# Performance work log

Hardware: AMD Instinct MI355X
Metric: run time of the kernel (lower is better)

## Reference

```python
import jax, jax.numpy as jnp
import numpy as np

M = 512          # feature_dim
NH = 8           # num_heads
FFN = 2048       # ffn_hidden_dim
NMOD = 4         # modalities (seq len for attention)
EPS = 1e-5


def setup_inputs() -> dict:
    key = jax.random.key(0)
    ks = jax.random.split(key, 16)
    B, H = 64, 256
    s = 0.02
    return {
        "x_image": jax.random.normal(ks[0], (B, H, M), jnp.float32),
        "x_radar": jax.random.normal(ks[1], (B, H, M), jnp.float32),
        "x_lidar": jax.random.normal(ks[2], (B, H, M), jnp.float32),
        "x_gps":   jax.random.normal(ks[3], (B, H, M), jnp.float32),
        # nn.MultiheadAttention params (torch layout: weight is (out,in))
        "in_proj_w": jax.random.normal(ks[4], (3 * M, M), jnp.float32) * s,
        "in_proj_b": jnp.zeros((3 * M,), jnp.float32),
        "out_proj_w": jax.random.normal(ks[5], (M, M), jnp.float32) * s,
        "out_proj_b": jnp.zeros((M,), jnp.float32),
        "ln1_g": jnp.ones((M,), jnp.float32),
        "ln1_b": jnp.zeros((M,), jnp.float32),
        "w1": jax.random.normal(ks[6], (FFN, M), jnp.float32) * s,
        "b1": jnp.zeros((FFN,), jnp.float32),
        "w2": jax.random.normal(ks[7], (M, FFN), jnp.float32) * s,
        "b2": jnp.zeros((M,), jnp.float32),
        "ln2_g": jnp.ones((M,), jnp.float32),
        "ln2_b": jnpp if False else jnp.zeros((M,), jnp.float32),
    }


def _layernorm(x, g, b):
    mu = jnp.mean(x, axis=-1, keepdims=True)
    var = jnp.mean((x - mu) ** 2, axis=-1, keepdims=True)
    return (x - mu) * jax.lax.rsqrt(var + EPS) * g + b


def _forward(x_image, x_radar, x_lidar, x_gps,
             in_proj_w, in_proj_b, out_proj_w, out_proj_b,
             ln1_g, ln1_b, w1, b1, w2, b2, ln2_g, ln2_b):
    B, H, _ = x_image.shape
    # F: (B*H, NMOD, M) -- fold batch and time; per-t loop is independent
    F = jnp.stack([x_image, x_radar, x_lidar, x_gps], axis=2).reshape(B * H, NMOD, M)
    qkv = F @ in_proj_w.T + in_proj_b              # (N, NMOD, 3M)
    q, k, v = jnp.split(qkv, 3, axis=-1)
    dh = M // NH
    def heads(t):  # (N, NMOD, M) -> (N, NH, NMOD, dh)
        return t.reshape(-1, NMOD, NH, dh).transpose(0, 2, 1, 3)
    qh, kh, vh = heads(q), heads(k), heads(v)
    scores = jnp.einsum("bhsd,bhtd->bhst", qh, kh) / np.sqrt(dh).astype(np.float32)
    attn = jax.nn.softmax(scores, axis=-1)
    o = jnp.einsum("bhst,bhtd->bhsd", attn, vh)
    o = o.transpose(0, 2, 1, 3).reshape(-1, NMOD, M)
    attn_out = o @ out_proj_w.T + out_proj_b
    h1 = _layernorm(F + attn_out, ln1_g, ln1_b)    # (N, NMOD, M)
    agg = h1.sum(axis=1)                            # (N, M)
    ffn = jax.nn.gelu(agg @ w1.T + b1, approximate=False) @ w2.T + b2
    z = _layernorm(agg + ffn, ln2_g, ln2_b)
    return z.reshape(B, H, M)


def reference(x_image, x_radar, x_lidar, x_gps,
              in_proj_w, in_proj_b, out_proj_w, out_proj_b,
              ln1_g, ln1_b, w1, b1, w2, b2, ln2_g, ln2_b):
    return _forward(x_image, x_radar, x_lidar, x_gps,
                    in_proj_w, in_proj_b, out_proj_w, out_proj_b,
                    ln1_g, ln1_b, w1, b1, w2, b2, ln2_g, ln2_b)
```

## Files before the change

kernel.cpp:

```cpp
#include <hip/hip_runtime.h>
#include <hip/hip_bf16.h>


typedef __attribute__((ext_vector_type(8))) short s16x8;
typedef __attribute__((ext_vector_type(4))) float f32x4;

__device__ __forceinline__ unsigned short f2bf(float f) {
  unsigned int u = __float_as_uint(f);
  u += 0x7fffu + ((u >> 16) & 1u);
  return (unsigned short)(u >> 16);
}
__device__ __forceinline__ float bf2f(unsigned short s) {
  return __uint_as_float(((unsigned int)s) << 16);
}
__device__ __forceinline__ f32x4 mfma16(s16x8 a, s16x8 b, f32x4 c) {
  return __builtin_amdgcn_mfma_f32_16x16x32_bf16(a, b, c, 0, 0, 0);
}
__device__ __forceinline__ int swz(int row, int bir) {
  return row * 128 + ((((row) & 7) << 4) ^ bir);
}
__device__ __forceinline__ int qkswz(int row, int c) {
  return row * 128 + ((((c >> 3) ^ (row & 7)) << 4)) + (c & 7) * 2;
}
__device__ __forceinline__ int vtswz(int d, int row) {
  return d * 256 + ((((row >> 3) ^ (d & 7)) << 4)) + (row & 7) * 2;
}
__device__ __forceinline__ int pwswz(int row, int c) {
  return row * 64 + ((((c >> 3) ^ (row & 3)) << 4)) + (c & 7) * 2;
}
__device__ __forceinline__ int vtoff(int r, int c) {
  return r * 1024 + ((c * 2) ^ ((r & 7) << 4));
}
__device__ __forceinline__ void gl_lds16(const void* g, void* l) {
  __builtin_amdgcn_global_load_lds(
      (const __attribute__((address_space(1))) unsigned int*)g,
      (__attribute__((address_space(3))) unsigned int*)l, 16, 0, 0);
}

__global__ void pack_kernel(const float* __restrict__ wqkv, const float* __restrict__ wout,
                            const float* __restrict__ w1, const float* __restrict__ w2,
                            const float* __restrict__ x0, const float* __restrict__ x1,
                            const float* __restrict__ x2, const float* __restrict__ x3,
                            unsigned short* __restrict__ o_wqkv, unsigned short* __restrict__ o_wout,
                            unsigned short* __restrict__ o_w1, unsigned short* __restrict__ o_w2,
                            unsigned short* __restrict__ o_x4) {
  const long c0 = 196608, c1 = 262144, c2 = 524288, c3 = 786432, c4 = 9175040;
  for (long v = (long)blockIdx.x * blockDim.x + threadIdx.x; v < c4;
       v += (long)gridDim.x * blockDim.x) {
    const float* src;
    unsigned short* dst;
    if (v < c0) { src = wqkv + v * 4; dst = o_wqkv + v * 4; }
    else if (v < c1) { long u = v - c0; src = wout + u * 4; dst = o_wout + u * 4; }
    else if (v < c2) { long u = v - c1; src = w1 + u * 4; dst = o_w1 + u * 4; }
    else if (v < c3) { long u = v - c2; src = w2 + u * 4; dst = o_w2 + u * 4; }
    else {
      long u = v - c3; long e = u * 4; long r = e >> 9; int i = (int)(e & 511);
      int s = (int)(r & 3); long n = r >> 2;
      const float* xs = (s == 0) ? x0 : (s == 1) ? x1 : (s == 2) ? x2 : x3;
      src = xs + n * 512 + i; dst = o_x4 + e;
    }
    float4 f = *reinterpret_cast<const float4*>(src);
    ushort4 hb;
    hb.x = f2bf(f.x); hb.y = f2bf(f.y); hb.z = f2bf(f.z); hb.w = f2bf(f.w);
    *reinterpret_cast<ushort4*>(dst) = hb;
  }
}

__launch_bounds__(256, 3)
__global__ void qkv_attn_kernel(const unsigned short* __restrict__ x4,
                                const unsigned short* __restrict__ wqkv,
                                const float* __restrict__ in_b,
                                unsigned short* __restrict__ o_out) {
  const int wg = blockIdx.x;
  const int slot = wg >> 3, xcd = wg & 7;
  const int tb = ((slot >> 3) << 3) | xcd;
  const int h = slot & 7;
  const int tid = threadIdx.x, lane = tid & 63, w = tid >> 6;
  const int wm = w >> 1, wn = w & 1;

  __shared__ __align__(16) unsigned char smem[49152];
  unsigned short* aT = (unsigned short*)smem;
  unsigned short* bT = (unsigned short*)(smem + 16384);
  unsigned short* Qs = (unsigned short*)smem;
  unsigned short* Ks = (unsigned short*)(smem + 16384);
  unsigned short* Vt = (unsigned short*)(smem + 32768);
  unsigned short* Pw = (unsigned short*)smem;
  unsigned short* outT = (unsigned short*)(smem + 16384);

  f32x4 acc[4][6];
#pragma unroll
  for (int i = 0; i < 4; ++i)
#pragma unroll
    for (int j = 0; j < 6; ++j) acc[i][j] = (f32x4){0.f, 0.f, 0.f, 0.f};

  const long rowBase = (long)tb * 128;
  const int loff = ((lane >> 3) * 512) + (((lane & 7) ^ (lane >> 3)) * 8);

  for (int kk = 0; kk < 8; ++kk) {
    const int k0 = kk * 64;
#pragma unroll
    for (int it = 0; it < 4; ++it) {
      int c = w * 4 + it;
      gl_lds16(x4 + (rowBase + c * 8) * 512 + k0 + loff, aT + c * 512);
    }
#pragma unroll
    for (int it = 0; it < 6; ++it) {
      int c = w * 6 + it;
      int bc0 = c * 8;
      int wb = (bc0 < 64) ? (h * 64 + bc0)
             : (bc0 < 128) ? (512 + h * 64 + (bc0 - 64))
                           : (1024 + h * 64 + (bc0 - 128));
      gl_lds16(wqkv + (long)wb * 512 + k0 + loff, bT + c * 512);
    }
    __syncthreads();
#pragma unroll
    for (int k2 = 0; k2 < 2; ++k2) {
      s16x8 af[4], bfr[6];
      const int bir = k2 * 64 + ((lane >> 4) << 4);
#pragma unroll
      for (int mi = 0; mi < 4; ++mi) {
        int row = wm * 64 + mi * 16 + (lane & 15);
        af[mi] = *(const s16x8*)((unsigned char*)aT + swz(row, bir));
      }
#pragma unroll
      for (int ni = 0; ni < 6; ++ni) {
        int col = wn * 96 + ni * 16 + (lane & 15);
        bfr[ni] = *(const s16x8*)((unsigned char*)bT + swz(col, bir));
      }
#pragma unroll
      for (int mi = 0; mi < 4; ++mi)
#pragma unroll
        for (int ni = 0; ni < 6; ++ni)
          acc[mi][ni] = mfma16(af[mi], bfr[ni], acc[mi][ni]);
    }
    __syncthreads();
  }

#pragma unroll
  for (int mi = 0; mi < 4; ++mi)
#pragma unroll
    for (int ni = 0; ni < 6; ++ni) {
      int col = wn * 96 + ni * 16 + (lane & 15);
      int wb = (col < 64) ? (h * 64 + col)
             : (col < 128) ? (512 + h * 64 + (col - 64))
                           : (1024 + h * 64 + (col - 128));
      float bias = in_b[wb];
      int row0 = wm * 64 + mi * 16 + ((lane >> 4) << 2);
#pragma unroll
      for (int r = 0; r < 4; ++r) {
        int row = row0 + r;
        unsigned short hv = f2bf(acc[mi][ni][r] + bias);
        if (col < 64)
          *(unsigned short*)((unsigned char*)Qs + qkswz(row, col)) = hv;
        else if (col < 128)
          *(unsigned short*)((unsigned char*)Ks + qkswz(row, col - 64)) = hv;
        else
          *(unsigned short*)((unsigned char*)Vt + vtswz(col - 128, row)) = hv;
      }
    }
  __syncthreads();

  f32x4 sacc[2];
#pragma unroll
  for (int i2 = 0; i2 < 2; ++i2) {
    int ti = w * 2 + i2;
    int qrow = ti * 16 + (lane & 15);
    int bir = (lane >> 4) << 4;
    s16x8 qa0 = *(const s16x8*)((unsigned char*)Qs + swz(qrow, bir));
    s16x8 qa1 = *(const s16x8*)((unsigned char*)Qs + swz(qrow, 64 + bir));
    s16x8 ka0 = *(const s16x8*)((unsigned char*)Ks + swz(qrow, bir));
    s16x8 ka1 = *(const s16x8*)((unsigned char*)Ks + swz(qrow, 64 + bir));
    f32x4 s = (f32x4){0.f, 0.f, 0.f, 0.f};
    s = mfma16(qa0, ka0, s);
    s = mfma16(qa1, ka1, s);
    sacc[i2] = s;
  }
  __syncthreads();
  {
    s16x8 z = (s16x8){0, 0, 0, 0, 0, 0, 0, 0};
    ((s16x8*)Pw)[tid] = z;
    ((s16x8*)Pw)[tid + 256] = z;
  }
  __syncthreads();

  const bool rel = ((lane & 15) >> 2) == (lane >> 4);
#pragma unroll
  for (int i2 = 0; i2 < 2; ++i2) {
    int ti = w * 2 + i2;
#pragma unroll
    for (int r = 0; r < 4; ++r) {
      float sc = sacc[i2][r] * 0.125f;
      float m = fmaxf(sc, __shfl_xor(sc, 1));
      m = fmaxf(m, __shfl_xor(m, 2));
      float e = __expf(sc - m);
      float su = e + __shfl_xor(e, 1);
      su = su + __shfl_xor(su, 2);
      float p = e / su;
      if (rel) {
        int row = ti * 16 + ((lane >> 4) << 2) + r;
        int cl = (((row >> 2) & 7) << 2) + (lane & 3);
        *(unsigned short*)((unsigned char*)Pw + pwswz(row, cl)) = f2bf(p);
      }
    }
  }
  __syncthreads();

#pragma unroll
  for (int i2 = 0; i2 < 2; ++i2) {
    int ti = w * 2 + i2;
    int arow = ti * 16 + (lane & 15);
    s16x8 pa = *(const s16x8*)((unsigned char*)Pw + arow * 64 +
                               ((((lane >> 4) ^ (arow & 3)) << 4)));
    f32x4 pv4[4];
#pragma unroll
    for (int n = 0; n < 4; ++n) {
      int d = n * 16 + (lane & 15);
      int gran = ((ti >> 1) << 2) + (lane >> 4);
      s16x8 vb = *(const s16x8*)((unsigned char*)Vt + d * 256 +
                                 (((gran ^ (d & 7)) << 4)));
      pv4[n] = mfma16(pa, vb, (f32x4){0.f, 0.f, 0.f, 0.f});
    }
#pragma unroll
    for (int n = 0; n < 4; ++n) {
      int d = n * 16 + (lane & 15);
      int row0 = ti * 16 + ((lane >> 4) << 2);
#pragma unroll
      for (int r = 0; r < 4; ++r)
        *(unsigned short*)((unsigned char*)outT + qkswz(row0 + r, d)) =
            f2bf(pv4[n][r]);
    }
  }
  __syncthreads();
#pragma unroll
  for (int j = 0; j < 4; ++j) {
    int c = j * 256 + tid;
    int row = c >> 3, ch = c & 7;
    s16x8 v = *(const s16x8*)((unsigned char*)outT + qkswz(row, ch * 8));
    *(s16x8*)(o_out + (rowBase + row) * 512 + h * 64 + ch * 8) = v;
  }
}

__launch_bounds__(256)
__global__ void outproj_ln1_kernel(const unsigned short* __restrict__ o_in,
                                   const unsigned short* __restrict__ wout,
                                   const float* __restrict__ out_b,
                                   const unsigned short* __restrict__ x4,
                                   const float* __restrict__ ln1_g, const float* __restrict__ ln1_b,
                                   float* __restrict__ agg_f, unsigned short* __restrict__ agg_b) {
  const int tb = blockIdx.x;
  const int tid = threadIdx.x, lane = tid & 63, w = tid >> 6;
  __shared__ __align__(16) unsigned char smem[53504];
  unsigned short* vt = (unsigned short*)smem;
  unsigned short* aT = (unsigned short*)(smem + 32768);
  unsigned short* bT = (unsigned short*)(smem + 36864);
  float* stats = (float*)(smem + 53248);
  const long rowBase = (long)tb * 32;

  for (int ns = 0; ns < 4; ++ns) {
    f32x4 acc[2][2];
#pragma unroll
    for (int i = 0; i < 2; ++i)
#pragma unroll
      for (int j = 0; j < 2; ++j) acc[i][j] = (f32x4){0.f, 0.f, 0.f, 0.f};
    for (int kk = 0; kk < 8; ++kk) {
      const int k0 = kk * 64;
      {
        int lr = tid >> 3, c8 = tid & 7;
        s16x8 v = *(const s16x8*)(o_in + (rowBase + lr) * 512 + k0 + c8 * 8);
        *(s16x8*)((unsigned char*)aT + swz(lr, c8 * 16)) = v;
      }
#pragma unroll
      for (int it = 0; it < 4; ++it) {
        int cid = tid + it * 256, bc = cid >> 3, c8 = cid & 7;
        s16x8 v = *(const s16x8*)(wout + (long)(ns * 128 + bc) * 512 + k0 + c8 * 8);
        *(s16x8*)((unsigned char*)bT + swz(bc, c8 * 16)) = v;
      }
      __syncthreads();
#pragma unroll
      for (int k2 = 0; k2 < 2; ++k2) {
        s16x8 af[2], bfr[2];
        const int bir = k2 * 64 + ((lane >> 4) << 4);
#pragma unroll
        for (int mi = 0; mi < 2; ++mi) {
          int row = mi * 16 + (lane & 15);
          af[mi] = *(const s16x8*)((unsigned char*)aT + swz(row, bir));
        }
#pragma unroll
        for (int ni = 0; ni < 2; ++ni) {
          int col = w * 32 + ni * 16 + (lane & 15);
          bfr[ni] = *(const s16x8*)((unsigned char*)bT + swz(col, bir));
        }
#pragma unroll
        for (int mi = 0; mi < 2; ++mi)
#pragma unroll
          for (int ni = 0; ni < 2; ++ni)
            acc[mi][ni] = mfma16(af[mi], bfr[ni], acc[mi][ni]);
      }
      __syncthreads();
    }
#pragma unroll
    for (int mi = 0; mi < 2; ++mi)
#pragma unroll
      for (int ni = 0; ni < 2; ++ni) {
        int gcol = ns * 128 + w * 32 + ni * 16 + (lane & 15);
        float bias = out_b[gcol];
        int row0 = mi * 16 + ((lane >> 4) << 2);
#pragma unroll
        for (int r = 0; r < 4; ++r) {
          int rr = row0 + r;
          float F = bf2f(x4[(rowBase + rr) * 512 + gcol]);
          *(unsigned short*)((unsigned char*)vt + vtoff(rr, gcol)) =
              f2bf(acc[mi][ni][r] + bias + F);
        }
      }
  }
  __syncthreads();
  {
    int wv = tid >> 6, ln = tid & 63;
    for (int i = 0; i < 8; ++i) {
      int r = wv * 8 + i;
      s16x8 v8 = *(const s16x8*)((unsigned char*)vt + vtoff(r, ln * 8));
      float sum = 0.f, sq = 0.f;
#pragma unroll
      for (int d = 0; d < 8; ++d) {
        float v = bf2f((unsigned short)v8[d]);
        sum += v; sq += v * v;
      }
#pragma unroll
      for (int off = 1; off < 64; off <<= 1) {
        sum += __shfl_xor(sum, off); sq += __shfl_xor(sq, off);
      }
      if (ln == 0) {
        float mu = sum * (1.f / 512.f);
        float var = sq * (1.f / 512.f) - mu * mu;
        stats[r * 2] = mu;
        stats[r * 2 + 1] = rsqrtf(var + 1e-5f);
      }
    }
  }
  __syncthreads();
  for (int it = 0; it < 2; ++it) {
    int ci = tid + it * 256;
    int tok = ci >> 6, c0 = (ci & 63) * 8;
    long gtok = (long)tb * 8 + tok;
    float a[8] = {0.f, 0.f, 0.f, 0.f, 0.f, 0.f, 0.f, 0.f};
#pragma unroll
    for (int s = 0; s < 4; ++s) {
      int r = tok * 4 + s;
      s16x8 v8 = *(const s16x8*)((unsigned char*)vt + vtoff(r, c0));
      float mu = stats[r * 2], is = stats[r * 2 + 1];
#pragma unroll
      for (int d = 0; d < 8; ++d) a[d] += (bf2f((unsigned short)v8[d]) - mu) * is;
    }
    float4 g0 = *(const float4*)(ln1_g + c0);
    float4 g1 = *(const float4*)(ln1_g + c0 + 4);
    float4 b0 = *(const float4*)(ln1_b + c0);
    float4 b1 = *(const float4*)(ln1_b + c0 + 4);
    float ov[8];
    ov[0] = g0.x * a[0] + 4.f * b0.x; ov[1] = g0.y * a[1] + 4.f * b0.y;
    ov[2] = g0.z * a[2] + 4.f * b0.z; ov[3] = g0.w * a[3] + 4.f * b0.w;
    ov[4] = g1.x * a[4] + 4.f * b1.x; ov[5] = g1.y * a[5] + 4.f * b1.y;
    ov[6] = g1.z * a[6] + 4.f * b1.z; ov[7] = g1.w * a[7] + 4.f * b1.w;
    *(float4*)(agg_f + gtok * 512 + c0) = (float4){ov[0], ov[1], ov[2], ov[3]};
    *(float4*)(agg_f + gtok * 512 + c0 + 4) = (float4){ov[4], ov[5], ov[6], ov[7]};
    s16x8 ab;
#pragma unroll
    for (int d = 0; d < 8; ++d) ab[d] = (short)f2bf(ov[d]);
    *(s16x8*)(agg_b + gtok * 512 + c0) = ab;
  }
}

__launch_bounds__(256)
__global__ void ffn1_kernel(const unsigned short* __restrict__ aggb,
                            const unsigned short* __restrict__ w1b,
                            const float* __restrict__ b1,
                            unsigned short* __restrict__ hidden) {
  const int wg = blockIdx.x;
  const int slot = wg >> 3, xcd = wg & 7;
  const int by = ((slot >> 4) << 3) | xcd;
  const int bx = slot & 15;
  const int tid = threadIdx.x, lane = tid & 63, w = tid >> 6;
  const int wm = w >> 1, wn = w & 1;
  __shared__ __align__(16) unsigned char smem[32768];
  unsigned short* aT = (unsigned short*)smem;
  unsigned short* bT = (unsigned short*)(smem + 16384);
  f32x4 acc[4][4];
#pragma unroll
  for (int i = 0; i < 4; ++i)
#pragma unroll
    for (int j = 0; j < 4; ++j) acc[i][j] = (f32x4){0.f, 0.f, 0.f, 0.f};
  const long rowBase = (long)by * 128;
  const long colBase = (long)bx * 128;
  const int loff = ((lane >> 3) * 512) + (((lane & 7) ^ (lane >> 3)) * 8);
  for (int kk = 0; kk < 8; ++kk) {
    const int k0 = kk * 64;
#pragma unroll
    for (int it = 0; it < 4; ++it) {
      int c = w * 4 + it;
      gl_lds16(aggb + (rowBase + c * 8) * 512 + k0 + loff, aT + c * 512);
    }
#pragma unroll
    for (int it = 0; it < 4; ++it) {
      int c = w * 4 + it;
      gl_lds16(w1b + (colBase + c * 8) * 512 + k0 + loff, bT + c * 512);
    }
    __syncthreads();
#pragma unroll
    for (int k2 = 0; k2 < 2; ++k2) {
      s16x8 af[4], bfr[4];
      const int bir = k2 * 64 + ((lane >> 4) << 4);
#pragma unroll
      for (int mi = 0; mi < 4; ++mi) {
        int row = wm * 64 + mi * 16 + (lane & 15);
        af[mi] = *(const s16x8*)((unsigned char*)aT + swz(row, bir));
      }
#pragma unroll
      for (int ni = 0; ni < 4; ++ni) {
        int col = wn * 64 + ni * 16 + (lane & 15);
        bfr[ni] = *(const s16x8*)((unsigned char*)bT + swz(col, bir));
      }
#pragma unroll
      for (int mi = 0; mi < 4; ++mi)
#pragma unroll
        for (int ni = 0; ni < 4; ++ni)
          acc[mi][ni] = mfma16(af[mi], bfr[ni], acc[mi][ni]);
    }
    __syncthreads();
  }
#pragma unroll
  for (int mi = 0; mi < 4; ++mi)
#pragma unroll
    for (int ni = 0; ni < 4; ++ni) {
      long gcol = colBase + wn * 64 + ni * 16 + (lane & 15);
      float bias = b1[gcol];
      int row0 = wm * 64 + mi * 16 + ((lane >> 4) << 2);
#pragma unroll
      for (int r = 0; r < 4; ++r) {
        float x = acc[mi][ni][r] + bias;
        float g = 0.5f * x * (1.f + erff(x * 0.70710678118f));
        hidden[(rowBase + row0 + r) * 2048 + gcol] = f2bf(g);
      }
    }
}

__launch_bounds__(256)
__global__ void ffn2_kernel(const unsigned short* __restrict__ hidden,
                            const unsigned short* __restrict__ w2b,
                            const float* __restrict__ b2,
                            const float* __restrict__ agg_f,
                            float* __restrict__ ffn2s) {
  const int wg = blockIdx.x;
  const int slot = wg >> 3, xcd = wg & 7;
  const int by = ((slot >> 2) << 3) | xcd;
  const int bx = slot & 3;
  const int tid = threadIdx.x, lane = tid & 63, w = tid >> 6;
  const int wm = w >> 1, wn = w & 1;
  __shared__ __align__(16) unsigned char smem[32768];
  unsigned short* aT = (unsigned short*)smem;
  unsigned short* bT = (unsigned short*)(smem + 16384);
  f32x4 acc[4][4];
#pragma unroll
  for (int i = 0; i < 4; ++i)
#pragma unroll
    for (int j = 0; j < 4; ++j) acc[i][j] = (f32x4){0.f, 0.f, 0.f, 0.f};
  const long rowBase = (long)by * 128;
  const long colBase = (long)bx * 128;
  const int loff2k = ((lane >> 3) * 2048) + (((lane & 7) ^ (lane >> 3)) * 8);
  for (int kk = 0; kk < 32; ++kk) {
    const int k0 = kk * 64;
#pragma unroll
    for (int it = 0; it < 4; ++it) {
      int c = w * 4 + it;
      gl_lds16(hidden + (rowBase + c * 8) * 2048 + k0 + loff2k, aT + c * 512);
    }
#pragma unroll
    for (int it = 0; it < 4; ++it) {
      int c = w * 4 + it;
      gl_lds16(w2b + (colBase + c * 8) * 2048 + k0 + loff2k, bT + c * 512);
    }
    __syncthreads();
#pragma unroll
    for (int k2 = 0; k2 < 2; ++k2) {
      s16x8 af[4], bfr[4];
      const int bir = k2 * 64 + ((lane >> 4) << 4);
#pragma unroll
      for (int mi = 0; mi < 4; ++mi) {
        int row = wm * 64 + mi * 16 + (lane & 15);
        af[mi] = *(const s16x8*)((unsigned char*)aT + swz(row, bir));
      }
#pragma unroll
      for (int ni = 0; ni < 4; ++ni) {
        int col = wn * 64 + ni * 16 + (lane & 15);
        bfr[ni] = *(const s16x8*)((unsigned char*)bT + swz(col, bir));
      }
#pragma unroll
      for (int mi = 0; mi < 4; ++mi)
#pragma unroll
        for (int ni = 0; ni < 4; ++ni)
          acc[mi][ni] = mfma16(af[mi], bfr[ni], acc[mi][ni]);
    }
    __syncthreads();
  }
#pragma unroll
  for (int mi = 0; mi < 4; ++mi)
#pragma unroll
    for (int ni = 0; ni < 4; ++ni) {
      long gcol = colBase + wn * 64 + ni * 16 + (lane & 15);
      float bias = b2[gcol];
      int row0 = wm * 64 + mi * 16 + ((lane >> 4) << 2);
#pragma unroll
      for (int r = 0; r < 4; ++r) {
        long grow = rowBase + row0 + r;
        ffn2s[grow * 512 + gcol] = acc[mi][ni][r] + bias + agg_f[grow * 512 + gcol];
      }
    }
}

__launch_bounds__(256)
__global__ void ln2_kernel(const float* __restrict__ ffn2s,
                           const float* __restrict__ ln2_g,
                           const float* __restrict__ ln2_b,
                           float* __restrict__ out) {
  const int tb = blockIdx.x;
  const int lane = threadIdx.x & 63, wv = threadIdx.x >> 6;
  const int c0 = lane * 8;
  float4 g0 = *(const float4*)(ln2_g + c0);
  float4 g1 = *(const float4*)(ln2_g + c0 + 4);
  float4 b0 = *(const float4*)(ln2_b + c0);
  float4 b1 = *(const float4*)(ln2_b + c0 + 4);
#pragma unroll
  for (int i = 0; i < 4; ++i) {
    long row = (long)tb * 16 + wv * 4 + i;
    const float* src = ffn2s + row * 512 + c0;
    float4 a = *(const float4*)src;
    float4 c = *(const float4*)(src + 4);
    float sum = a.x + a.y + a.z + a.w + c.x + c.y + c.z + c.w;
    float sq = a.x * a.x + a.y * a.y + a.z * a.z + a.w * a.w +
               c.x * c.x + c.y * c.y + c.z * c.z + c.w * c.w;
#pragma unroll
    for (int off = 1; off < 64; off <<= 1) {
      sum += __shfl_xor(sum, off); sq += __shfl_xor(sq, off);
    }
    float mu = sum * (1.f / 512.f);
    float is = rsqrtf(sq * (1.f / 512.f) - mu * mu + 1e-5f);
    float* dst = out + row * 512 + c0;
    *(float4*)dst = (float4){(a.x - mu) * is * g0.x + b0.x, (a.y - mu) * is * g0.y + b0.y,
                             (a.z - mu) * is * g0.z + b0.z, (a.w - mu) * is * g0.w + b0.w};
    *(float4*)(dst + 4) = (float4){(c.x - mu) * is * g1.x + b1.x, (c.y - mu) * is * g1.y + b1.y,
                                   (c.z - mu) * is * g1.z + b1.z, (c.w - mu) * is * g1.w + b1.w};
  }
}

extern "C" void kernel_launch(void* const* d_in, const int* in_sizes, int n_in,
                              void* d_out, int out_size, void* d_ws, size_t ws_size,
                              hipStream_t stream) {
  (void)in_sizes; (void)n_in; (void)out_size;
  const float* x0 = (const float*)d_in[0];
  const float* x1 = (const float*)d_in[1];
  const float* x2 = (const float*)d_in[2];
  const float* x3 = (const float*)d_in[3];
  const float* in_w = (const float*)d_in[4];
  const float* in_b = (const float*)d_in[5];
  const float* out_w = (const float*)d_in[6];
  const float* out_b = (const float*)d_in[7];
  const float* ln1_g = (const float*)d_in[8];
  const float* ln1_b = (const float*)d_in[9];
  const float* w1 = (const float*)d_in[10];
  const float* b1 = (const float*)d_in[11];
  const float* w2 = (const float*)d_in[12];
  const float* b2 = (const float*)d_in[13];
  const float* ln2_g = (const float*)d_in[14];
  const float* ln2_b = (const float*)d_in[15];
  float* out = (float*)d_out;

  unsigned char* ws = (unsigned char*)d_ws;
  if (ws_size < 190840832u) return;
  unsigned short* wqkv_b = (unsigned short*)(ws + 0);
  unsigned short* wout_b = (unsigned short*)(ws + 1572864);
  unsigned short* w1_b = (unsigned short*)(ws + 2097152);
  unsigned short* w2_b = (unsigned short*)(ws + 4194304);
  unsigned short* x4 = (unsigned short*)(ws + 6291456);
  unsigned short* o_buf = (unsigned short*)(ws + 73400320);
  float* agg_f = (float*)(ws + 140509184);
  unsigned short* agg_b = (unsigned short*)(ws + 174063616);
  unsigned short* hidden = o_buf;
  float* ffn2s = (float*)(ws + 6291456);

  pack_kernel<<<2048, 256, 0, stream>>>(in_w, out_w, w1, w2, x0, x1, x2, x3,
                                        wqkv_b, wout_b, w1_b, w2_b, x4);
  qkv_attn_kernel<<<4096, 256, 0, stream>>>(x4, wqkv_b, in_b, o_buf);
  outproj_ln1_kernel<<<2048, 256, 0, stream>>>(o_buf, wout_b, out_b, x4,
                                               ln1_g, ln1_b, agg_f, agg_b);
  ffn1_kernel<<<2048, 256, 0, stream>>>(agg_b, w1_b, b1, hidden);
  ffn2_kernel<<<512, 256, 0, stream>>>(hidden, w2_b, b2, agg_f, ffn2s);
  ln2_kernel<<<1024, 256, 0, stream>>>(ffn2s, ln2_g, ln2_b, out);
}
```

Baseline: 394.6 us.

## Fuse input fp32-to-bf16 conversion into QKV attention load and drop x4 buffer

Removes packing of the four modality inputs into an interleaved bf16 buffer. The QKV/attention kernel now reads fp32 inputs directly and converts to bf16 while staging into LDS, and the out-projection epilogue reads the fp32 residual directly. This saves a full write and read pass over a large intermediate. In exchange, each head block re-reads twice as many bytes per x tile, and the x loads become synchronous register loads instead of direct-to-LDS loads.

```diff
diff --git a/kernel.cpp b/kernel.cpp
--- a/kernel.cpp
+++ b/kernel.cpp
@@ -37,28 +37,19 @@
       (__attribute__((address_space(3))) unsigned int*)l, 16, 0, 0);
 }
 
-__global__ void pack_kernel(const float* __restrict__ wqkv, const float* __restrict__ wout,
-                            const float* __restrict__ w1, const float* __restrict__ w2,
-                            const float* __restrict__ x0, const float* __restrict__ x1,
-                            const float* __restrict__ x2, const float* __restrict__ x3,
-                            unsigned short* __restrict__ o_wqkv, unsigned short* __restrict__ o_wout,
-                            unsigned short* __restrict__ o_w1, unsigned short* __restrict__ o_w2,
-                            unsigned short* __restrict__ o_x4) {
-  const long c0 = 196608, c1 = 262144, c2 = 524288, c3 = 786432, c4 = 9175040;
-  for (long v = (long)blockIdx.x * blockDim.x + threadIdx.x; v < c4;
+__global__ void pack_w_kernel(const float* __restrict__ wqkv, const float* __restrict__ wout,
+                              const float* __restrict__ w1, const float* __restrict__ w2,
+                              unsigned short* __restrict__ o_wqkv, unsigned short* __restrict__ o_wout,
+                              unsigned short* __restrict__ o_w1, unsigned short* __restrict__ o_w2) {
+  const long c0 = 196608, c1 = 262144, c2 = 524288, c3 = 786432;
+  for (long v = (long)blockIdx.x * blockDim.x + threadIdx.x; v < c3;
        v += (long)gridDim.x * blockDim.x) {
     const float* src;
     unsigned short* dst;
     if (v < c0) { src = wqkv + v * 4; dst = o_wqkv + v * 4; }
     else if (v < c1) { long u = v - c0; src = wout + u * 4; dst = o_wout + u * 4; }
     else if (v < c2) { long u = v - c1; src = w1 + u * 4; dst = o_w1 + u * 4; }
-    else if (v < c3) { long u = v - c2; src = w2 + u * 4; dst = o_w2 + u * 4; }
-    else {
-      long u = v - c3; long e = u * 4; long r = e >> 9; int i = (int)(e & 511);
-      int s = (int)(r & 3); long n = r >> 2;
-      const float* xs = (s == 0) ? x0 : (s == 1) ? x1 : (s == 2) ? x2 : x3;
-      src = xs + n * 512 + i; dst = o_x4 + e;
-    }
+    else { long u = v - c2; src = w2 + u * 4; dst = o_w2 + u * 4; }
     float4 f = *reinterpret_cast<const float4*>(src);
     ushort4 hb;
     hb.x = f2bf(f.x); hb.y = f2bf(f.y); hb.z = f2bf(f.z); hb.w = f2bf(f.w);
@@ -67,7 +58,8 @@
 }
 
 __launch_bounds__(256, 3)
-__global__ void qkv_attn_kernel(const unsigned short* __restrict__ x4,
+__global__ void qkv_attn_kernel(const float* __restrict__ x0, const float* __restrict__ x1,
+                                const float* __restrict__ x2, const float* __restrict__ x3,
                                 const unsigned short* __restrict__ wqkv,
                                 const float* __restrict__ in_b,
                                 unsigned short* __restrict__ o_out) {
@@ -94,15 +86,12 @@
     for (int j = 0; j < 6; ++j) acc[i][j] = (f32x4){0.f, 0.f, 0.f, 0.f};
 
   const long rowBase = (long)tb * 128;
+  const long tokBase = (long)tb * 32;
   const int loff = ((lane >> 3) * 512) + (((lane & 7) ^ (lane >> 3)) * 8);
+  const float* xs[4] = {x0, x1, x2, x3};
 
   for (int kk = 0; kk < 8; ++kk) {
     const int k0 = kk * 64;
-#pragma unroll
-    for (int it = 0; it < 4; ++it) {
-      int c = w * 4 + it;
-      gl_lds16(x4 + (rowBase + c * 8) * 512 + k0 + loff, aT + c * 512);
-    }
 #pragma unroll
     for (int it = 0; it < 6; ++it) {
       int c = w * 6 + it;
@@ -111,6 +100,21 @@
              : (bc0 < 128) ? (512 + h * 64 + (bc0 - 64))
                            : (1024 + h * 64 + (bc0 - 128));
       gl_lds16(wqkv + (long)wb * 512 + k0 + loff, bT + c * 512);
+    }
+#pragma unroll
+    for (int it = 0; it < 4; ++it) {
+      int cid = tid + it * 256, lr = cid >> 3, c8 = cid & 7;
+      int s = lr & 3;
+      long n = tokBase + (lr >> 2);
+      const float* src = xs[s] + n * 512 + k0 + c8 * 8;
+      float4 f0 = *(const float4*)src;
+      float4 f1 = *(const float4*)(src + 4);
+      s16x8 v;
+      v[0] = (short)f2bf(f0.x); v[1] = (short)f2bf(f0.y);
+      v[2] = (short)f2bf(f0.z); v[3] = (short)f2bf(f0.w);
+      v[4] = (short)f2bf(f1.x); v[5] = (short)f2bf(f1.y);
+      v[6] = (short)f2bf(f1.z); v[7] = (short)f2bf(f1.w);
+      *(s16x8*)((unsigned char*)aT + swz(lr, c8 * 16)) = v;
     }
     __syncthreads();
 #pragma unroll
@@ -244,7 +248,8 @@
 __global__ void outproj_ln1_kernel(const unsigned short* __restrict__ o_in,
                                    const unsigned short* __restrict__ wout,
                                    const float* __restrict__ out_b,
-                                   const unsigned short* __restrict__ x4,
+                                   const float* __restrict__ x0, const float* __restrict__ x1,
+                                   const float* __restrict__ x2, const float* __restrict__ x3,
                                    const float* __restrict__ ln1_g, const float* __restrict__ ln1_b,
                                    float* __restrict__ agg_f, unsigned short* __restrict__ agg_b) {
   const int tb = blockIdx.x;
@@ -255,6 +260,7 @@
   unsigned short* bT = (unsigned short*)(smem + 36864);
   float* stats = (float*)(smem + 53248);
   const long rowBase = (long)tb * 32;
+  const float* xs[4] = {x0, x1, x2, x3};
 
   for (int ns = 0; ns < 4; ++ns) {
     f32x4 acc[2][2];
@@ -308,7 +314,9 @@
 #pragma unroll
         for (int r = 0; r < 4; ++r) {
           int rr = row0 + r;
-          float F = bf2f(x4[(rowBase + rr) * 512 + gcol]);
+          long grow = rowBase + rr;
+          int s = (int)(grow & 3); long n = grow >> 2;
+          float F = xs[s][n * 512 + gcol];
           *(unsigned short*)((unsigned char*)vt + vtoff(rr, gcol)) =
               f2bf(acc[mi][ni][r] + bias + F);
         }
@@ -579,17 +587,16 @@
   unsigned short* wout_b = (unsigned short*)(ws + 1572864);
   unsigned short* w1_b = (unsigned short*)(ws + 2097152);
   unsigned short* w2_b = (unsigned short*)(ws + 4194304);
-  unsigned short* x4 = (unsigned short*)(ws + 6291456);
+  float* ffn2s = (float*)(ws + 6291456);
   unsigned short* o_buf = (unsigned short*)(ws + 73400320);
   float* agg_f = (float*)(ws + 140509184);
   unsigned short* agg_b = (unsigned short*)(ws + 174063616);
   unsigned short* hidden = o_buf;
-  float* ffn2s = (float*)(ws + 6291456);
-
-  pack_kernel<<<2048, 256, 0, stream>>>(in_w, out_w, w1, w2, x0, x1, x2, x3,
-                                        wqkv_b, wout_b, w1_b, w2_b, x4);
-  qkv_attn_kernel<<<4096, 256, 0, stream>>>(x4, wqkv_b, in_b, o_buf);
-  outproj_ln1_kernel<<<2048, 256, 0, stream>>>(o_buf, wout_b, out_b, x4,
+
+  pack_w_kernel<<<1024, 256, 0, stream>>>(in_w, out_w, w1, w2,
+                                          wqkv_b, wout_b, w1_b, w2_b);
+  qkv_attn_kernel<<<4096, 256, 0, stream>>>(x0, x1, x2, x3, wqkv_b, in_b, o_buf);
+  outproj_ln1_kernel<<<2048, 256, 0, stream>>>(o_buf, wout_b, out_b, x0, x1, x2, x3,
                                                ln1_g, ln1_b, agg_f, agg_b);
   ffn1_kernel<<<2048, 256, 0, stream>>>(agg_b, w1_b, b1, hidden);
   ffn2_kernel<<<512, 256, 0, stream>>>(hidden, w2_b, b2, agg_f, ffn2s);
```

New measurement: 464.6 us. +17.7%, slower.
